# Kernel tuning notes

Measured on AMD Instinct MI355X. Metric: run time of the kernel, lower is better.

## Reference

```python
import math
import jax, jax.numpy as jnp
import numpy as np

H, W = 512, 512            # volume_shape
N_ANGLES = 360
N_DET = 736                # num_detectors
DET_SPACING = 1.0          # detector_spacing (voxel units)
STEP = 1.0                 # ray-marching step (voxel units)
N_STEPS = int(math.ceil(math.hypot(H, W)))  # 725 samples along each ray


def setup_inputs() -> dict:
    key = jax.random.key(0)
    k1, k2 = jax.random.split(key)
    x = jax.random.normal(k1, (H, W), dtype=jnp.float32)
    # learned reconstruction parameter (zeros in the module; small randn here so the add is non-trivial)
    reco = jax.random.normal(k2, (H, W), dtype=jnp.float32) * 0.1
    angles = jnp.linspace(0.0, np.pi, N_ANGLES, endpoint=False, dtype=jnp.float32)
    return {"x": x, "reco": reco, "angles": angles}


def _bilinear(img, xs, ys):
    """Bilinear interpolation of img[y, x] with zero padding outside."""
    h, w = img.shape
    x0 = jnp.floor(xs)
    y0 = jnp.floor(ys)
    wx = xs - x0
    wy = ys - y0
    x0i = x0.astype(jnp.int32)
    y0i = y0.astype(jnp.int32)

    def fetch(yi, xi):
        inb = (xi >= 0) & (xi < w) & (yi >= 0) & (yi < h)
        v = img[jnp.clip(yi, 0, h - 1), jnp.clip(xi, 0, w - 1)]
        return jnp.where(inb, v, jnp.zeros((), img.dtype))

    return (fetch(y0i, x0i) * (1 - wx) * (1 - wy)
            + fetch(y0i, x0i + 1) * wx * (1 - wy)
            + fetch(y0i + 1, x0i) * (1 - wx) * wy
            + fetch(y0i + 1, x0i + 1) * wx * wy)


def _radon(img, angles):
    """Parallel-beam ray-driven forward projection -> sinogram (n_angles, n_det)."""
    cx = (W - 1) * 0.5
    cy = (H - 1) * 0.5
    u = (jnp.arange(N_DET, dtype=img.dtype) - (N_DET - 1) * 0.5) * DET_SPACING
    t = (jnp.arange(N_STEPS, dtype=img.dtype) - (N_STEPS - 1) * 0.5) * STEP

    def one_angle(theta):
        c = jnp.cos(theta)
        s = jnp.sin(theta)
        # ray: p(t) = u * perp + t * dir, dir = (c, s), perp = (-s, c); centered on volume
        xs = -s * u[:, None] + c * t[None, :] + cx   # (D, T)
        ys = c * u[:, None] + s * t[None, :] + cy    # (D, T)
        return _bilinear(img, xs, ys).sum(axis=1) * STEP  # (D,)

    # lax.map keeps per-angle intermediates small (ray-driven accumulation)
    return jax.lax.map(one_angle, angles)  # (A, D)


def reference(x, reco, angles):
    updated_reco = x + reco
    current_sino = _radon(updated_reco, angles)
    return current_sino, updated_reco
```

## Files before the change

### kernel.cpp

```cpp
#include <hip/hip_runtime.h>
#include <math.h>

constexpr int H = 512, W = 512;
constexpr int N_ANGLES = 360;
constexpr int N_DET = 736;
constexpr int N_STEPS = 725;
constexpr int SINO_SIZE = N_ANGLES * N_DET;

constexpr int THREADS  = 256;
constexpr int DET_TILE = 64;
constexpr int K_TILE   = 32;
constexpr int PITCH    = 84;
constexpr int ROWS     = 75;
constexpr int QCHUNKS  = PITCH / 4;
constexpr int MAXJ     = 7;

constexpr int PADX = 96, PADY = 96;
constexpr int PW = 720;
constexpr int PH = 704;
constexpr size_t PAD_BYTES = (size_t)PW * PH * 4;

typedef float v2f __attribute__((ext_vector_type(2)));

__global__ void pad_kernel(const float* __restrict__ x,
                           const float* __restrict__ reco,
                           float* __restrict__ padded,
                           float* __restrict__ updated) {
    int i = blockIdx.x * blockDim.x + threadIdx.x;
    if (i >= PW * PH) return;
    int p = i / PW, q = i - p * PW;
    int gy = p - PADY, gx = q - PADX;
    float v = 0.0f;
    if ((unsigned)gy < (unsigned)H && (unsigned)gx < (unsigned)W) {
        int gi = gy * W + gx;
        v = x[gi] + reco[gi];
        updated[gi] = v;
    }
    padded[i] = v;
}

__global__ void add_kernel(const float4* __restrict__ x,
                           const float4* __restrict__ reco,
                           float4* __restrict__ out) {
    int i = blockIdx.x * blockDim.x + threadIdx.x;
    float4 a = x[i];
    float4 b = reco[i];
    out[i] = make_float4(a.x + b.x, a.y + b.y, a.z + b.z, a.w + b.w);
}

template <bool DMA>
__global__ __launch_bounds__(THREADS, 6) void radon_kernel(const float* __restrict__ img,
                                                           const float* __restrict__ angles,
                                                           float* __restrict__ sino) {
    __shared__ float tile[ROWS * PITCH];

    const int tid = threadIdx.x;
    const int w   = tid >> 6;
    const int l   = tid & 63;
    const int dt_ = 16 * w + (l & 15);
    const int klr = l >> 4;
    const int a   = blockIdx.y;
    const int d0  = blockIdx.x * DET_TILE;

    const float theta = angles[a];
    const float c = cosf(theta);
    const float s = sinf(theta);
    const float ac = fabsf(c), as = fabsf(s);
    const float cx = (W - 1) * 0.5f;
    const float cy = (H - 1) * 0.5f;
    const float t_off = (N_STEPS - 1) * 0.5f;

    const float u   = (float)(d0 + dt_) - (N_DET - 1) * 0.5f;
    const float bxu = cx - s * u;
    const float byu = cy + c * u;

    const float uLo = (float)d0 - (N_DET - 1) * 0.5f;
    const float uHi = uLo + (DET_TILE - 1);
    float su0 = s * uLo, su1 = s * uHi;
    float smin = fminf(su0, su1), smax = fmaxf(su0, su1);
    float cu0 = c * uLo, cu1 = c * uHi;
    float cmin = fminf(cu0, cu1), cmax = fmaxf(cu0, cu1);

    float tmin = -1e30f, tmax = 1e30f;
    {
        float xlo = -1.0f - cx + smin;
        float xhi = (float)W - cx + smax;
        if (ac > 1e-12f) {
            float t0 = xlo / c, t1 = xhi / c;
            tmin = fmaxf(tmin, fminf(t0, t1));
            tmax = fminf(tmax, fmaxf(t0, t1));
        } else if (xlo > 0.0f || xhi < 0.0f) {
            tmax = -2e30f;
        }
    }
    {
        float ylo = -1.0f - cy - cmax;
        float yhi = (float)H - cy - cmin;
        if (as > 1e-12f) {
            float t0 = ylo / s, t1 = yhi / s;
            tmin = fmaxf(tmin, fminf(t0, t1));
            tmax = fminf(tmax, fmaxf(t0, t1));
        } else if (ylo > 0.0f || yhi < 0.0f) {
            tmax = -2e30f;
        }
    }
    int kminU = (int)fminf(725.0f, fmaxf(0.0f, ceilf(tmin + t_off) - 1.0f));
    int kmaxU = (int)fmaxf(-1.0f, fminf((float)(N_STEPS - 1), floorf(tmax + t_off) + 1.0f));
    if (kminU > kmaxU) { kminU = N_STEPS; kmaxU = -1; }

    const float ucf = uLo + 0.5f * (DET_TILE - 1);
    const v2f dinc = {4.0f * c, 4.0f * s};

    float acc = 0.0f;

    for (int k0 = kminU; k0 <= kmaxU; k0 += K_TILE) {
        const int k1 = min(k0 + K_TILE - 1, kmaxU);
        const float t0f = (float)k0 - t_off;
        const float dt  = (float)(k1 - k0);
        const float tc  = t0f + 0.5f * dt;
        const float xc_ = fmaf(c, tc, cx) - s * ucf;
        const float yc_ = fmaf(s, tc, cy) + c * ucf;
        const float hx = fmaf(0.5f * ac, dt, 0.5f * (DET_TILE - 1) * as) + 0.5f;
        const float hy = fmaf(0.5f * as, dt, 0.5f * (DET_TILE - 1) * ac) + 0.5f;
        int x0 = ((int)floorf(xc_ - hx)) & ~3;
        int y0 = (int)floorf(yc_ - hy);
        x0 = min(max(x0, -PADX), PW - PADX - PITCH);
        y0 = min(max(y0, -PADY), PH - PADY - ROWS);
        const int bh = min((int)floorf(yc_ + hy) + 2 - y0, ROWS);

        if constexpr (DMA) {
            const int total = bh * QCHUNKS;
            const float* srow = img + (size_t)(y0 + PADY) * PW + (x0 + PADX);
            #pragma unroll
            for (int j = 0; j < MAXJ; ++j) {
                const int i = tid + j * THREADS;
                if (i < total) {
                    const int r  = i / QCHUNKS;
                    const int ch = i - r * QCHUNKS;
                    const float* src = srow + r * PW + ch * 4;
                    float* dst = tile + (size_t)(i & ~63) * 4;
                    __builtin_amdgcn_global_load_lds(
                        (const __attribute__((address_space(1))) unsigned*)src,
                        (__attribute__((address_space(3))) unsigned*)dst,
                        16, 0, 0);
                }
            }
        } else {
            const int total = bh * PITCH;
            for (int i = tid; i < total; i += THREADS) {
                int r  = i / PITCH;
                int gxx = i - r * PITCH + x0;
                int gy = y0 + r;
                float v = 0.0f;
                if ((unsigned)gxx < (unsigned)W && (unsigned)gy < (unsigned)H)
                    v = img[gy * W + gxx];
                tile[i] = v;
            }
        }
        __syncthreads();

        const int kst = k0 + klr;
        v2f pos = {fmaf(c, (float)kst - t_off, bxu) - (float)x0,
                   fmaf(s, (float)kst - t_off, byu) - (float)y0};
        #pragma unroll 4
        for (int k = kst; k <= k1; k += 4) {
            int xi = (int)pos.x;
            int yi = (int)pos.y;
            float wx = __builtin_amdgcn_fractf(pos.x);
            float wy = __builtin_amdgcn_fractf(pos.y);
            int idx = __mul24(yi, PITCH) + xi;
            v2f c0 = {tile[idx],     tile[idx + PITCH]};
            v2f c1 = {tile[idx + 1], tile[idx + PITCH + 1]};
            v2f diff = c1 - c0;
            v2f wx2 = {wx, wx};
            v2f tb = __builtin_elementwise_fma(wx2, diff, c0);
            acc = fmaf(wy, tb.y - tb.x, acc + tb.x);
            pos += dinc;
        }
        __syncthreads();
    }

    acc += __shfl_xor(acc, 16);
    acc += __shfl_xor(acc, 32);
    if (l < 16) {
        int d = d0 + 16 * w + l;
        if (d < N_DET) sino[a * N_DET + d] = acc;
    }
}

extern "C" void kernel_launch(void* const* d_in, const int* in_sizes, int n_in,
                              void* d_out, int out_size, void* d_ws, size_t ws_size,
                              hipStream_t stream) {
    const float* x      = (const float*)d_in[0];
    const float* reco   = (const float*)d_in[1];
    const float* angles = (const float*)d_in[2];

    float* sino    = (float*)d_out;
    float* updated = (float*)d_out + SINO_SIZE;

    dim3 grid((N_DET + DET_TILE - 1) / DET_TILE, N_ANGLES);

    if (ws_size >= PAD_BYTES) {
        float* padded = (float*)d_ws;
        pad_kernel<<<(PW * PH + 255) / 256, 256, 0, stream>>>(x, reco, padded, updated);
        radon_kernel<true><<<grid, THREADS, 0, stream>>>(padded, angles, sino);
    } else {
        int n4 = (H * W) / 4;
        add_kernel<<<n4 / 256, 256, 0, stream>>>(
            (const float4*)x, (const float4*)reco, (float4*)updated);
        radon_kernel<false><<<grid, THREADS, 0, stream>>>(updated, angles, sino);
    }
}
```

Measured before the change: 101.1 us.

## Give each wavefront a private LDS tile and drop block barriers

```diff
diff --git a/kernel.cpp b/kernel.cpp
--- a/kernel.cpp
+++ b/kernel.cpp
@@ -7,13 +7,14 @@
 constexpr int N_STEPS = 725;
 constexpr int SINO_SIZE = N_ANGLES * N_DET;
 
-constexpr int THREADS  = 256;
-constexpr int DET_TILE = 64;
-constexpr int K_TILE   = 32;
-constexpr int PITCH    = 84;
-constexpr int ROWS     = 75;
-constexpr int QCHUNKS  = PITCH / 4;
-constexpr int MAXJ     = 7;
+constexpr int THREADS   = 256;
+constexpr int WAVE_DETS = 16;
+constexpr int K_TILE    = 32;
+constexpr int PITCH     = 44;
+constexpr int ROWS      = 38;
+constexpr int QCHUNKS   = PITCH / 4;
+constexpr int TILE_DW   = ROWS * PITCH;
+constexpr int MAXJ      = 7;
 
 constexpr int PADX = 96, PADY = 96;
 constexpr int PW = 720;
@@ -52,15 +53,17 @@
 __global__ __launch_bounds__(THREADS, 6) void radon_kernel(const float* __restrict__ img,
                                                            const float* __restrict__ angles,
                                                            float* __restrict__ sino) {
-    __shared__ float tile[ROWS * PITCH];
+    __shared__ float tiles[4][TILE_DW];
 
     const int tid = threadIdx.x;
     const int w   = tid >> 6;
     const int l   = tid & 63;
-    const int dt_ = 16 * w + (l & 15);
+    float* tile = tiles[w];
+
+    const int dt_ = l & 15;
     const int klr = l >> 4;
     const int a   = blockIdx.y;
-    const int d0  = blockIdx.x * DET_TILE;
+    const int d0w = blockIdx.x * 64 + w * WAVE_DETS;
 
     const float theta = angles[a];
     const float c = cosf(theta);
@@ -70,12 +73,12 @@
     const float cy = (H - 1) * 0.5f;
     const float t_off = (N_STEPS - 1) * 0.5f;
 
-    const float u   = (float)(d0 + dt_) - (N_DET - 1) * 0.5f;
+    const float u   = (float)(d0w + dt_) - (N_DET - 1) * 0.5f;
     const float bxu = cx - s * u;
     const float byu = cy + c * u;
 
-    const float uLo = (float)d0 - (N_DET - 1) * 0.5f;
-    const float uHi = uLo + (DET_TILE - 1);
+    const float uLo = (float)d0w - (N_DET - 1) * 0.5f;
+    const float uHi = uLo + (WAVE_DETS - 1);
     float su0 = s * uLo, su1 = s * uHi;
     float smin = fminf(su0, su1), smax = fmaxf(su0, su1);
     float cu0 = c * uLo, cu1 = c * uHi;
@@ -108,7 +111,7 @@
     int kmaxU = (int)fmaxf(-1.0f, fminf((float)(N_STEPS - 1), floorf(tmax + t_off) + 1.0f));
     if (kminU > kmaxU) { kminU = N_STEPS; kmaxU = -1; }
 
-    const float ucf = uLo + 0.5f * (DET_TILE - 1);
+    const float ucf = uLo + 0.5f * (WAVE_DETS - 1);
     const v2f dinc = {4.0f * c, 4.0f * s};
 
     float acc = 0.0f;
@@ -120,8 +123,8 @@
         const float tc  = t0f + 0.5f * dt;
         const float xc_ = fmaf(c, tc, cx) - s * ucf;
         const float yc_ = fmaf(s, tc, cy) + c * ucf;
-        const float hx = fmaf(0.5f * ac, dt, 0.5f * (DET_TILE - 1) * as) + 0.5f;
-        const float hy = fmaf(0.5f * as, dt, 0.5f * (DET_TILE - 1) * ac) + 0.5f;
+        const float hx = fmaf(0.5f * ac, dt, 0.5f * (WAVE_DETS - 1) * as) + 0.5f;
+        const float hy = fmaf(0.5f * as, dt, 0.5f * (WAVE_DETS - 1) * ac) + 0.5f;
         int x0 = ((int)floorf(xc_ - hx)) & ~3;
         int y0 = (int)floorf(yc_ - hy);
         x0 = min(max(x0, -PADX), PW - PADX - PITCH);
@@ -133,21 +136,22 @@
             const float* srow = img + (size_t)(y0 + PADY) * PW + (x0 + PADX);
             #pragma unroll
             for (int j = 0; j < MAXJ; ++j) {
-                const int i = tid + j * THREADS;
+                const int i = l + j * 64;
                 if (i < total) {
                     const int r  = i / QCHUNKS;
                     const int ch = i - r * QCHUNKS;
                     const float* src = srow + r * PW + ch * 4;
-                    float* dst = tile + (size_t)(i & ~63) * 4;
+                    float* dst = tile + (size_t)(j * 64) * 4;
                     __builtin_amdgcn_global_load_lds(
                         (const __attribute__((address_space(1))) unsigned*)src,
                         (__attribute__((address_space(3))) unsigned*)dst,
                         16, 0, 0);
                 }
             }
+            asm volatile("s_waitcnt vmcnt(0)" ::: "memory");
         } else {
             const int total = bh * PITCH;
-            for (int i = tid; i < total; i += THREADS) {
+            for (int i = l; i < total; i += 64) {
                 int r  = i / PITCH;
                 int gxx = i - r * PITCH + x0;
                 int gy = y0 + r;
@@ -157,7 +161,6 @@
                 tile[i] = v;
             }
         }
-        __syncthreads();
 
         const int kst = k0 + klr;
         v2f pos = {fmaf(c, (float)kst - t_off, bxu) - (float)x0,
@@ -177,13 +180,12 @@
             acc = fmaf(wy, tb.y - tb.x, acc + tb.x);
             pos += dinc;
         }
-        __syncthreads();
     }
 
     acc += __shfl_xor(acc, 16);
     acc += __shfl_xor(acc, 32);
-    if (l < 16) {
-        int d = d0 + 16 * w + l;
+    if (l < WAVE_DETS) {
+        int d = d0w + l;
         if (d < N_DET) sino[a * N_DET + d] = acc;
     }
 }
@@ -198,7 +200,7 @@
     float* sino    = (float*)d_out;
     float* updated = (float*)d_out + SINO_SIZE;
 
-    dim3 grid((N_DET + DET_TILE - 1) / DET_TILE, N_ANGLES);
+    dim3 grid((N_DET + 63) / 64, N_ANGLES);
 
     if (ws_size >= PAD_BYTES) {
         float* padded = (float*)d_ws;
```

Result: faster. 98.64 us (-2.4%).
